# Performance work log

Measured on AMD Instinct MI355X. Metric: run time of the kernel, lower is better.

Reference implementation:

```python
import jax, jax.numpy as jnp
import numpy as np

TEMPERATURE = 0.5
NEG_INF_FILL = -1000000000.0


def setup_inputs() -> dict:
    key = jax.random.key(0)
    z = jax.random.normal(key, (16384, 128), dtype=jnp.float32)
    # module expects L2-normalized projected features
    z = z / jnp.linalg.norm(z, axis=-1, keepdims=True)
    return {"z": z}


def reference(z) -> jnp.ndarray:
    N2 = z.shape[0]
    N = N2 // 2
    # (2N, 2N) pairwise similarity scaled by temperature
    sim = (z @ z.T) / TEMPERATURE
    # mask self-similarity on the diagonal
    eye = jnp.eye(N2, dtype=bool)
    sim = jnp.where(eye, NEG_INF_FILL, sim)
    # positive pair index: row i < N pairs with i+N; row i >= N pairs with i-N
    pos_idx = jnp.concatenate([jnp.arange(N, N2), jnp.arange(0, N)])
    positives = sim[jnp.arange(N2), pos_idx]
    loss = -positives + jax.scipy.special.logsumexp(sim, axis=1)
    return loss.mean()
```

## Files before the change

### kernel.cpp

```cpp
#include <hip/hip_runtime.h>
#include <hip/hip_bf16.h>

#define N2    16384
#define NHALF 8192
#define KDIM  128
#define BROW  128
#define BCOL  256
#define NQUARTER 4096
#define NITER (NQUARTER / BCOL)

using bf16x8 = __attribute__((ext_vector_type(8))) short;
using f32x4  = __attribute__((ext_vector_type(4))) float;

#if __has_builtin(__builtin_amdgcn_exp2f)
#define EXP2F(x) __builtin_amdgcn_exp2f(x)
#else
#define EXP2F(x) exp2f(x)
#endif
#if __has_builtin(__builtin_amdgcn_logf)
#define LOG2F(x) __builtin_amdgcn_logf(x)
#else
#define LOG2F(x) log2f(x)
#endif

#define PRESCALE 1.6986436005760381f

typedef const __attribute__((address_space(1))) void* gas_ptr;
typedef __attribute__((address_space(3))) void* las_ptr;

__device__ __forceinline__ unsigned short f2bf(float f) {
  unsigned u = __float_as_uint(f);
  u += 0x7fffu + ((u >> 16) & 1u);
  return (unsigned short)(u >> 16);
}

__global__ void k_convert(const float* __restrict__ z, unsigned short* __restrict__ zb,
                          float* __restrict__ S, float* __restrict__ out) {
  int i = blockIdx.x * blockDim.x + threadIdx.x;
  if (i < N2) S[i] = 0.f;
  if (i == 0) out[0] = 0.f;
  float4 v = reinterpret_cast<const float4*>(z)[i];
  ushort4 o;
  o.x = f2bf(v.x * PRESCALE); o.y = f2bf(v.y * PRESCALE);
  o.z = f2bf(v.z * PRESCALE); o.w = f2bf(v.w * PRESCALE);
  reinterpret_cast<ushort4*>(zb)[i] = o;
}

__global__ __launch_bounds__(512, 2) void k_main(const unsigned short* __restrict__ zb,
                                                 float* __restrict__ S) {
  __shared__ __align__(16) unsigned short Bs[2][BCOL * KDIM];
  const int t    = threadIdx.x;
  const int w    = t >> 6;
  const int l    = t & 63;
  const int q    = l >> 4;
  const int c15  = l & 15;
  const int bt      = blockIdx.x >> 2;
  const int quarter = blockIdx.x & 3;
  const int mg   = w >> 2;
  const int ns   = w & 3;
  const int rbase = bt * BROW + mg * 64;

  int srcoff[8];
#pragma unroll
  for (int j = 0; j < 8; ++j) {
    int p   = (w * 8 + j) * 64 + l;
    int row = p >> 4;
    int pg  = p & 15;
    int k8  = pg ^ (row & 15);
    srcoff[j] = (row * 16 + k8) * 16;
  }

  const char* tile0 = (const char*)zb + (size_t)(quarter * NQUARTER) * KDIM * 2;

#pragma unroll
  for (int j = 0; j < 8; ++j)
    __builtin_amdgcn_global_load_lds((gas_ptr)(tile0 + srcoff[j]),
                                     (las_ptr)(&Bs[0][(w * 8 + j) * 512]), 16, 0, 0);

  bf16x8 afr[4][4];
#pragma unroll
  for (int m = 0; m < 4; ++m) {
    const unsigned short* ap = zb + (size_t)(rbase + m * 16 + c15) * KDIM + q * 8;
#pragma unroll
    for (int s = 0; s < 4; ++s)
      afr[m][s] = *reinterpret_cast<const bf16x8*>(ap + s * 32);
  }

  float rowsum[4][4];
#pragma unroll
  for (int m = 0; m < 4; ++m)
#pragma unroll
    for (int r = 0; r < 4; ++r) rowsum[m][r] = 0.f;

  for (int it = 0; it < NITER; ++it) {
    const int buf = it & 1;
    const int C0  = quarter * NQUARTER + it * BCOL;
    __syncthreads();

    if (it + 1 < NITER) {
      const char* src = tile0 + (size_t)(it + 1) * BCOL * KDIM * 2;
#pragma unroll
      for (int j = 0; j < 8; ++j)
        __builtin_amdgcn_global_load_lds((gas_ptr)(src + srcoff[j]),
                                         (las_ptr)(&Bs[buf ^ 1][(w * 8 + j) * 512]), 16, 0, 0);
    }

    f32x4 acc[4][4];
#pragma unroll
    for (int m = 0; m < 4; ++m)
#pragma unroll
      for (int n = 0; n < 4; ++n) acc[m][n] = (f32x4){0.f, 0.f, 0.f, 0.f};

#pragma unroll
    for (int s = 0; s < 4; ++s) {
      bf16x8 bfr[4];
#pragma unroll
      for (int n = 0; n < 4; ++n) {
        int rloc = ns * 64 + n * 16 + c15;
        int pg   = (s * 4 + q) ^ (rloc & 15);
        bfr[n] = *reinterpret_cast<const bf16x8*>(&Bs[buf][rloc * KDIM + pg * 8]);
      }
#pragma unroll
      for (int m = 0; m < 4; ++m)
#pragma unroll
        for (int n = 0; n < 4; ++n)
          acc[m][n] = __builtin_amdgcn_mfma_f32_16x16x32_bf16(afr[m][s], bfr[n], acc[m][n], 0, 0, 0);
    }

    const bool diagTile = (C0 + ns * 64) == rbase;
    if (diagTile) {
#pragma unroll
      for (int m = 0; m < 4; ++m)
#pragma unroll
        for (int n = 0; n < 4; ++n)
#pragma unroll
          for (int r = 0; r < 4; ++r) {
            float e = EXP2F(acc[m][n][r]);
            if ((m == n) && (c15 == q * 4 + r)) e = 0.f;
            rowsum[m][r] += e;
          }
    } else {
#pragma unroll
      for (int m = 0; m < 4; ++m)
#pragma unroll
        for (int n = 0; n < 4; ++n)
#pragma unroll
          for (int r = 0; r < 4; ++r) {
            rowsum[m][r] += EXP2F(acc[m][n][r]);
          }
    }
  }

#pragma unroll
  for (int m = 0; m < 4; ++m)
#pragma unroll
    for (int r = 0; r < 4; ++r) {
      float v = rowsum[m][r];
      v += __shfl_xor(v, 1);
      v += __shfl_xor(v, 2);
      v += __shfl_xor(v, 4);
      v += __shfl_xor(v, 8);
      if (c15 == 0) atomicAdd(&S[rbase + m * 16 + q * 4 + r], v);
    }
}

__global__ void k_final(const float* __restrict__ z, const float* __restrict__ S,
                        float* __restrict__ out) {
  __shared__ float red[256];
  int t = threadIdx.x;
  int i = blockIdx.x * 256 + t;
  int j = i ^ NHALF;
  const float4* zi = reinterpret_cast<const float4*>(z + (size_t)i * KDIM);
  const float4* zj = reinterpret_cast<const float4*>(z + (size_t)j * KDIM);
  float dot = 0.f;
#pragma unroll
  for (int k = 0; k < KDIM / 4; ++k) {
    float4 a = zi[k], b = zj[k];
    dot += a.x * b.x + a.y * b.y + a.z * b.z + a.w * b.w;
  }
  float loss = LOG2F(S[i]) * 0.69314718055994531f - 2.f * dot;
  red[t] = loss;
  __syncthreads();
  for (int o = 128; o > 0; o >>= 1) {
    if (t < o) red[t] += red[t + o];
    __syncthreads();
  }
  if (t == 0) atomicAdd(out, red[0] * (1.f / N2));
}

extern "C" void kernel_launch(void* const* d_in, const int* in_sizes, int n_in,
                              void* d_out, int out_size, void* d_ws, size_t ws_size,
                              hipStream_t stream) {
  const float* z = (const float*)d_in[0];
  float* out = (float*)d_out;
  unsigned short* zb = (unsigned short*)d_ws;
  float* S = (float*)((char*)d_ws + (size_t)N2 * KDIM * 2);

  k_convert<<<(N2 * KDIM / 4) / 256, 256, 0, stream>>>(z, zb, S, out);
  k_main<<<512, 512, 0, stream>>>(zb, S);
  k_final<<<N2 / 256, 256, 0, stream>>>(z, S, out);
}
```

Before: 140.4 us.

## Halve column tile and process MFMA output in 16-column slices

Shrinks the B column tile from 256 to 128, which halves LDS use per block (64KB double-buffered instead of 128KB), and restructures the inner loop so each wave handles 2 slices of 16 columns. Each slice uses only 4 accumulators instead of 16, with the diagonal mask checked per 16x16 block. The aim is lower register and LDS pressure so the launch bound of 2 blocks per CU can hold, and to interleave exp work with MFMA. In exchange there are twice as many iterations and barriers, and each LDS B fragment is reused across fewer MFMAs.

```diff
diff --git a/kernel.cpp b/kernel.cpp
--- a/kernel.cpp
+++ b/kernel.cpp
@@ -5,7 +5,7 @@
 #define NHALF 8192
 #define KDIM  128
 #define BROW  128
-#define BCOL  256
+#define BCOL  128
 #define NQUARTER 4096
 #define NITER (NQUARTER / BCOL)
 
@@ -60,10 +60,10 @@
   const int ns   = w & 3;
   const int rbase = bt * BROW + mg * 64;
 
-  int srcoff[8];
+  int srcoff[4];
 #pragma unroll
-  for (int j = 0; j < 8; ++j) {
-    int p   = (w * 8 + j) * 64 + l;
+  for (int j = 0; j < 4; ++j) {
+    int p   = (w * 4 + j) * 64 + l;
     int row = p >> 4;
     int pg  = p & 15;
     int k8  = pg ^ (row & 15);
@@ -73,9 +73,9 @@
   const char* tile0 = (const char*)zb + (size_t)(quarter * NQUARTER) * KDIM * 2;
 
 #pragma unroll
-  for (int j = 0; j < 8; ++j)
+  for (int j = 0; j < 4; ++j)
     __builtin_amdgcn_global_load_lds((gas_ptr)(tile0 + srcoff[j]),
-                                     (las_ptr)(&Bs[0][(w * 8 + j) * 512]), 16, 0, 0);
+                                     (las_ptr)(&Bs[0][(w * 4 + j) * 512]), 16, 0, 0);
 
   bf16x8 afr[4][4];
 #pragma unroll
@@ -100,54 +100,40 @@
     if (it + 1 < NITER) {
       const char* src = tile0 + (size_t)(it + 1) * BCOL * KDIM * 2;
 #pragma unroll
-      for (int j = 0; j < 8; ++j)
+      for (int j = 0; j < 4; ++j)
         __builtin_amdgcn_global_load_lds((gas_ptr)(src + srcoff[j]),
-                                         (las_ptr)(&Bs[buf ^ 1][(w * 8 + j) * 512]), 16, 0, 0);
+                                         (las_ptr)(&Bs[buf ^ 1][(w * 4 + j) * 512]), 16, 0, 0);
     }
 
-    f32x4 acc[4][4];
 #pragma unroll
-    for (int m = 0; m < 4; ++m)
+    for (int nt = 0; nt < 2; ++nt) {
+      const int rloc = ns * 32 + nt * 16 + c15;
+      f32x4 acc[4];
 #pragma unroll
-      for (int n = 0; n < 4; ++n) acc[m][n] = (f32x4){0.f, 0.f, 0.f, 0.f};
-
+      for (int m = 0; m < 4; ++m) acc[m] = (f32x4){0.f, 0.f, 0.f, 0.f};
 #pragma unroll
-    for (int s = 0; s < 4; ++s) {
-      bf16x8 bfr[4];
+      for (int s = 0; s < 4; ++s) {
+        int pg = (s * 4 + q) ^ (rloc & 15);
+        bf16x8 bfr = *reinterpret_cast<const bf16x8*>(&Bs[buf][rloc * KDIM + pg * 8]);
 #pragma unroll
-      for (int n = 0; n < 4; ++n) {
-        int rloc = ns * 64 + n * 16 + c15;
-        int pg   = (s * 4 + q) ^ (rloc & 15);
-        bfr[n] = *reinterpret_cast<const bf16x8*>(&Bs[buf][rloc * KDIM + pg * 8]);
+        for (int m = 0; m < 4; ++m)
+          acc[m] = __builtin_amdgcn_mfma_f32_16x16x32_bf16(afr[m][s], bfr, acc[m], 0, 0, 0);
       }
+      const int gcol = C0 + ns * 32 + nt * 16;
 #pragma unroll
-      for (int m = 0; m < 4; ++m)
-#pragma unroll
-        for (int n = 0; n < 4; ++n)
-          acc[m][n] = __builtin_amdgcn_mfma_f32_16x16x32_bf16(afr[m][s], bfr[n], acc[m][n], 0, 0, 0);
-    }
-
-    const bool diagTile = (C0 + ns * 64) == rbase;
-    if (diagTile) {
-#pragma unroll
-      for (int m = 0; m < 4; ++m)
-#pragma unroll
-        for (int n = 0; n < 4; ++n)
+      for (int m = 0; m < 4; ++m) {
+        if (gcol == rbase + m * 16) {
 #pragma unroll
           for (int r = 0; r < 4; ++r) {
-            float e = EXP2F(acc[m][n][r]);
-            if ((m == n) && (c15 == q * 4 + r)) e = 0.f;
+            float e = EXP2F(acc[m][r]);
+            if (c15 == q * 4 + r) e = 0.f;
             rowsum[m][r] += e;
           }
-    } else {
+        } else {
 #pragma unroll
-      for (int m = 0; m < 4; ++m)
-#pragma unroll
-        for (int n = 0; n < 4; ++n)
-#pragma unroll
-          for (int r = 0; r < 4; ++r) {
-            rowsum[m][r] += EXP2F(acc[m][n][r]);
-          }
+          for (int r = 0; r < 4; ++r) rowsum[m][r] += EXP2F(acc[m][r]);
+        }
+      }
     }
   }
 
```

Result: slower. 150.7 us (+7.4%).
